# Optimization experiments

Hardware: AMD Instinct MI355X
Metric: run time of the kernel (lower is better)

Reference implementation:

```python
import jax, jax.numpy as jnp
import numpy as np

B, S, D, H = 2, 2048, 1024, 16
HD = D // H  # 64
MASK_VAL = -10000.0


def setup_inputs() -> dict:
    key = jax.random.key(0)
    ks = jax.random.split(key, 8)
    sc = 0.02
    q_features = jax.random.normal(ks[0], (B, S, D), jnp.float32)
    kv_features = jax.random.normal(ks[1], (B, S, D), jnp.float32)
    # causal mask, broadcastable (1,1,S,S)
    mask = jnp.tril(jnp.ones((S, S), jnp.bool_))[None, None]
    Wq = jax.random.normal(ks[2], (D, D), jnp.float32) * sc
    bq = jnp.zeros((D,), jnp.float32)
    Wkv = jax.random.normal(ks[3], (D, 2 * D), jnp.float32) * sc
    bkv = jnp.zeros((2 * D,), jnp.float32)
    Wp = jax.random.normal(ks[4], (D, D), jnp.float32) * sc
    bp = jnp.zeros((D,), jnp.float32)
    return {"q_features": q_features, "kv_features": kv_features, "mask": mask,
            "Wq": Wq, "bq": bq, "Wkv": Wkv, "bkv": bkv, "Wp": Wp, "bp": bp}


def _split_heads(t):
    # (B,S,D) -> (B,H,S,HD)
    return t.reshape(B, S, H, HD).transpose(0, 2, 1, 3)


def reference(q_features, kv_features, mask, Wq, bq, Wkv, bkv, Wp, bp):
    query = q_features @ Wq + bq            # (B,S,D)
    kv = kv_features @ Wkv + bkv            # (B,S,2D)
    key, value = jnp.split(kv, 2, axis=-1)
    q = _split_heads(query)                 # (B,H,S,HD)
    k = _split_heads(key)
    v = _split_heads(value)
    scores = jnp.einsum('bhqd,bhkd->bhqk', q, k) / jnp.sqrt(jnp.float32(HD))
    scores = jnp.where(mask, scores, jnp.asarray(MASK_VAL, scores.dtype))
    attn = jax.nn.softmax(scores, axis=-1)  # (B,H,S,S)
    out = jnp.einsum('bhqk,bhkd->bhqd', attn, v)
    out = out.transpose(0, 2, 1, 3).reshape(B, S, D)  # merge heads
    return out @ Wp + bp
```

## Files before the change

kernel.cpp:

```cpp
#include <hip/hip_runtime.h>

typedef unsigned short u16;
typedef unsigned int u32;
typedef __attribute__((ext_vector_type(4))) unsigned short us4;
typedef __attribute__((ext_vector_type(8))) unsigned short us8;
typedef __attribute__((ext_vector_type(4))) short s16x4;
typedef __attribute__((ext_vector_type(8))) __bf16 bf16x8;
typedef __attribute__((ext_vector_type(4))) float floatx4;

#define S_ 2048
#define D_ 1024
#define QSC 0.18033688f

__device__ __forceinline__ float b2f(u16 u) {
  unsigned v = ((unsigned)u) << 16;
  return __builtin_bit_cast(float, v);
}
__device__ __forceinline__ u16 f2bf(float f) {
  unsigned u = __builtin_bit_cast(unsigned, f);
  unsigned r = (u + 0x7fffu + ((u >> 16) & 1u)) >> 16;
  return (u16)r;
}
__device__ __forceinline__ u16 f2bf_rhu(float f) {
  return (u16)((__builtin_bit_cast(unsigned, f) + 0x8000u) >> 16);
}

typedef const __attribute__((address_space(1))) u32* gas_t;
typedef __attribute__((address_space(3))) u32* las_t;
__device__ __forceinline__ void gload16(const u16* g, u16* l) {
  __builtin_amdgcn_global_load_lds((gas_t)g, (las_t)l, 16, 0, 0);
}

#define PBAR()                                   \
  {                                              \
    __builtin_amdgcn_sched_barrier(0);           \
    asm volatile("" ::: "memory");               \
    __builtin_amdgcn_s_barrier();                \
    asm volatile("" ::: "memory");               \
    __builtin_amdgcn_sched_barrier(0);           \
  }
#define WAITVM(N) asm volatile("s_waitcnt vmcnt(" #N ")" ::: "memory")

__global__ __launch_bounds__(256) void prep(
    const float* __restrict__ qf, const float* __restrict__ kvf,
    const float* __restrict__ Wq, const float* __restrict__ Wkv,
    const float* __restrict__ Wp, u16* __restrict__ qa, u16* __restrict__ kva,
    u16* __restrict__ Wqt, u16* __restrict__ Wkvt, u16* __restrict__ Wpt) {
  int bid = blockIdx.x, tid = threadIdx.x;
  if (bid < 4096) {
    const float* src = (bid < 2048) ? qf : kvf;
    u16* dst = (bid < 2048) ? qa : kva;
    size_t i = ((size_t)(bid & 2047) * 256 + tid) * 8;
    floatx4 a = *(const floatx4*)(src + i);
    floatx4 b = *(const floatx4*)(src + i + 4);
    us8 r;
#pragma unroll
    for (int j = 0; j < 4; j++) { r[j] = f2bf(a[j]); r[4 + j] = f2bf(b[j]); }
    *(us8*)(dst + i) = r;
  } else {
    int t = bid - 4096;
    const float* src; u16* dst; int R, C;
    if (t < 1024)      { src = Wq;  dst = Wqt;  R = 1024; C = 1024; }
    else if (t < 3072) { t -= 1024; src = Wkv; dst = Wkvt; R = 1024; C = 2048; }
    else               { t -= 3072; src = Wp;  dst = Wpt;  R = 1024; C = 1024; }
    int bx = t % (C >> 5), by = t / (C >> 5);
    __shared__ u16 tile[32][33];
    int tx = tid & 31, ty = tid >> 5;
    int x = bx * 32 + tx;
    for (int i = ty; i < 32; i += 8)
      tile[i][tx] = f2bf(src[(size_t)(by * 32 + i) * C + x]);
    __syncthreads();
    int r = tid >> 3, c4 = tid & 7;
    us4 v;
#pragma unroll
    for (int j = 0; j < 4; j++) v[j] = tile[c4 * 4 + j][r];
    *(us4*)&dst[(size_t)(bx * 32 + r) * R + by * 32 + c4 * 4] = v;
  }
}

template <int MODE>
__device__ __forceinline__ void gemm256(
    const u16* __restrict__ A, const u16* __restrict__ Bt,
    const float* __restrict__ bias, void* __restrict__ C0,
    u16* __restrict__ C1, int N, int m0, int n0, u16* smem, float cscale) {
  int tid = threadIdx.x;
  int w = tid >> 6, lane = tid & 63;
  int quad = lane >> 4, l16 = lane & 15;
  int wr = w >> 2, wc = w & 3;

  int srow = w * 32 + (lane >> 2);
  int gchunk = ((lane & 3) ^ ((lane >> 3) & 3)) << 3;
  const u16* Asrc = A + (size_t)(m0 + srow) * 1024 + gchunk;
  const u16* Bsrc = Bt + (size_t)(n0 + srow) * 1024 + gchunk;
  u16* Adst = smem + w * 1024;
  u16* Bdst = smem + 32768 + w * 1024;

  int swz = (quad ^ ((l16 >> 1) & 3)) << 3;
  int aoff = (wr * 128 + l16) * 32 + swz;
  int boff = 32768 + (wc * 64 + l16) * 32 + swz;

  floatx4 acc[8][4] = {};

#define STG(t)                                                 \
  {                                                            \
    int s_ = (t) & 3;                                          \
    gload16(Asrc + (t) * 32, Adst + s_ * 8192);                \
    gload16(Asrc + (t) * 32 + 16384, Adst + s_ * 8192 + 512);  \
    gload16(Bsrc + (t) * 32, Bdst + s_ * 8192);                \
    gload16(Bsrc + (t) * 32 + 16384, Bdst + s_ * 8192 + 512);  \
  }

  STG(0); STG(1); STG(2);
  WAITVM(8);
  PBAR();

#pragma unroll 1
  for (int t = 0; t < 32; t++) {
    int so = (t & 3) * 8192;
    bf16x8 af[8], bf[4];
#pragma unroll
    for (int mf = 0; mf < 8; mf++)
      af[mf] = __builtin_bit_cast(bf16x8,
          *(const us8*)&smem[so + aoff + mf * 512]);
#pragma unroll
    for (int nf = 0; nf < 4; nf++)
      bf[nf] = __builtin_bit_cast(bf16x8,
          *(const us8*)&smem[so + boff + nf * 512]);
    if (t < 29) STG(t + 3);
    __builtin_amdgcn_s_setprio(1);
#pragma unroll
    for (int mf = 0; mf < 8; mf++)
#pragma unroll
      for (int nf = 0; nf < 4; nf++)
        acc[mf][nf] = __builtin_amdgcn_mfma_f32_16x16x32_bf16(
            af[mf], bf[nf], acc[mf][nf], 0, 0, 0);
    __builtin_amdgcn_s_setprio(0);
    if (t < 29)      { WAITVM(8); }
    else if (t == 29){ WAITVM(4); }
    else if (t == 30){ WAITVM(0); }
    if (t < 31) PBAR();
  }
#undef STG

#pragma unroll
  for (int mf = 0; mf < 8; mf++) {
#pragma unroll
    for (int nf = 0; nf < 4; nf++) {
      int col = n0 + wc * 64 + nf * 16 + l16;
      int rowq = m0 + wr * 128 + mf * 16 + quad * 4;
      float bv = bias[col];
      if (MODE == 0) {
        u16* o = (u16*)C0;
#pragma unroll
        for (int r = 0; r < 4; r++)
          o[(size_t)(rowq + r) * N + col] = f2bf((acc[mf][nf][r] + bv) * cscale);
      } else {
        if (col < 1024) {
          u16* o = (u16*)C0;
#pragma unroll
          for (int r = 0; r < 4; r++)
            o[(size_t)(rowq + r) * 1024 + col] = f2bf(acc[mf][nf][r] + bv);
        } else {
          int vcol = col - 1024;
          int b = rowq >> 11, s0 = rowq & 2047;
          us4 pv;
#pragma unroll
          for (int r = 0; r < 4; r++) pv[r] = f2bf(acc[mf][nf][r] + bv);
          *(us4*)&C1[((size_t)(b * 1024 + vcol)) * (size_t)S_ + s0] = pv;
        }
      }
    }
  }
}

__global__ __launch_bounds__(512, 2) void gemm_qkv(
    const u16* __restrict__ qa, const u16* __restrict__ kva,
    const u16* __restrict__ Wqt, const u16* __restrict__ Wkvt,
    const float* __restrict__ bq, const float* __restrict__ bkv,
    u16* __restrict__ Qb, u16* __restrict__ Kb, u16* __restrict__ Vt) {
  __shared__ __align__(16) u16 smem[65536];
  int bid = blockIdx.x;
  int work = (bid & 7) * 24 + (bid >> 3);
  if (work < 64) {
    gemm256<0>(qa, Wqt, bq, Qb, nullptr, 1024,
               (work >> 2) * 256, (work & 3) * 256, smem, QSC);
  } else {
    int lb = work - 64;
    gemm256<2>(kva, Wkvt, bkv, Kb, Vt, 2048,
               (lb >> 3) * 256, (lb & 7) * 256, smem, 1.0f);
  }
}

template <int TM, int TN, int MODE>
__device__ __forceinline__ void gemm4w(
    const u16* __restrict__ A, const u16* __restrict__ Bt,
    const float* __restrict__ bias, void* __restrict__ C0,
    u16* __restrict__ C1, int N, int m0, int n0, u16* smem, float cscale) {
  constexpr int MF = TM / 32, NF = TN / 32;
  constexpr int ASZ = TM * 64;
  constexpr int SLOT = (TM + TN) * 64;
  int tid = threadIdx.x;
  int w = tid >> 6, lane = tid & 63;
  int quad = lane >> 4, l16 = lane & 15;
  int wr = w >> 1, wc = w & 1;

  int gch = ((lane & 7) ^ ((lane >> 3) & 7)) << 3;
  const u16* Ag = A + (size_t)(m0 + w * (TM / 4) + (lane >> 3)) * 1024 + gch;
  const u16* Bg = Bt + (size_t)(n0 + w * (TN / 4) + (lane >> 3)) * 1024 + gch;
  u16* Adst = smem + w * (TM / 4) * 64;
  u16* Bdst = smem + ASZ + w * (TN / 4) * 64;

  int ab = (wr * (TM / 2) + l16) * 64;
  int bb = ASZ + (wc * (TN / 2) + l16) * 64;
  int xk0 = (quad ^ (l16 & 7)) << 3;
  int xk1 = ((4 + quad) ^ (l16 & 7)) << 3;

  floatx4 acc[MF][NF] = {};

#define STAGE4(tn, s_)                                                  \
  {                                                                     \
    _Pragma("unroll") for (int i = 0; i < MF; i++)                      \
      gload16(Ag + (size_t)(tn) * 64 + (size_t)i * 8192,                \
              Adst + (s_) * SLOT + i * 512);                            \
    _Pragma("unroll") for (int i = 0; i < NF; i++)                      \
      gload16(Bg + (size_t)(tn) * 64 + (size_t)i * 8192,                \
              Bdst + (s_) * SLOT + i * 512);                            \
  }

#define COMPUTE4(SOFF)                                                  \
  {                                                                     \
    _Pragma("unroll") for (int kk = 0; kk < 2; kk++) {                  \
      int xk = kk ? xk1 : xk0;                                          \
      bf16x8 bfr[NF];                                                   \
      _Pragma("unroll") for (int nf = 0; nf < NF; nf++)                 \
        bfr[nf] = __builtin_bit_cast(bf16x8,                            \
            *(const us8*)&smem[(SOFF) + bb + nf * 1024 + xk]);          \
      _Pragma("unroll") for (int mf = 0; mf < MF; mf++) {               \
        bf16x8 afr = __builtin_bit_cast(bf16x8,                         \
            *(const us8*)&smem[(SOFF) + ab + mf * 1024 + xk]);          \
        _Pragma("unroll") for (int nf = 0; nf < NF; nf++)               \
          acc[mf][nf] = __builtin_amdgcn_mfma_f32_16x16x32_bf16(        \
              afr, bfr[nf], acc[mf][nf], 0, 0, 0);                      \
      }                                                                 \
    }                                                                   \
  }

  STAGE4(0, 0);
  WAITVM(0);
  PBAR();
#pragma unroll 1
  for (int t = 0; t < 16; t += 2) {
    STAGE4(t + 1, 1);
    COMPUTE4(0);
    WAITVM(0);
    PBAR();
    if (t + 2 < 16) STAGE4(t + 2, 0);
    COMPUTE4(SLOT);
    WAITVM(0);
    PBAR();
  }

#undef STAGE4
#undef COMPUTE4

#pragma unroll
  for (int mf = 0; mf < MF; mf++) {
#pragma unroll
    for (int nf = 0; nf < NF; nf++) {
      int col = n0 + wc * (TN / 2) + nf * 16 + l16;
      int rowq = m0 + wr * (TM / 2) + mf * 16 + quad * 4;
      float bv = bias[col];
      if (MODE == 0) {
        u16* o = (u16*)C0;
#pragma unroll
        for (int r = 0; r < 4; r++)
          o[(size_t)(rowq + r) * N + col] = f2bf((acc[mf][nf][r] + bv) * cscale);
      } else if (MODE == 1) {
        float* o = (float*)C0;
#pragma unroll
        for (int r = 0; r < 4; r++)
          o[(size_t)(rowq + r) * N + col] = acc[mf][nf][r] + bv;
      } else {
        if (col < 1024) {
          u16* o = (u16*)C0;
#pragma unroll
          for (int r = 0; r < 4; r++)
            o[(size_t)(rowq + r) * 1024 + col] = f2bf(acc[mf][nf][r] + bv);
        } else {
          int vcol = col - 1024;
          int b = rowq >> 11, s0 = rowq & 2047;
          us4 pv;
#pragma unroll
          for (int r = 0; r < 4; r++) pv[r] = f2bf(acc[mf][nf][r] + bv);
          *(us4*)&C1[((size_t)(b * 1024 + vcol)) * (size_t)S_ + s0] = pv;
        }
      }
    }
  }
}

__global__ __launch_bounds__(256, 3) void gemm_out(
    const u16* __restrict__ AO, const u16* __restrict__ Wpt,
    const float* __restrict__ bp, float* __restrict__ out) {
  __shared__ __align__(16) u16 smem[24576];
  int work = (blockIdx.x & 7) * 64 + (blockIdx.x >> 3);
  gemm4w<128, 64, 1>(AO, Wpt, bp, out, nullptr, 1024,
                     (work >> 4) * 128, (work & 15) * 64, smem, 1.0f);
}

__global__ __launch_bounds__(512, 4) void attn_fwd(
    const u16* __restrict__ Q, const u16* __restrict__ Kb,
    const u16* __restrict__ Vt, u16* __restrict__ O,
    u16* __restrict__ Opart, float* __restrict__ ml) {
  __shared__ __align__(16) u16 sm[16384];
  int tid  = threadIdx.x;
  int w    = tid >> 6, lane = tid & 63;
  int quad = lane >> 4, l16 = lane & 15;
  int bh = blockIdx.x, b = bh >> 4, h = bh & 15;
  int y = blockIdx.y;

  static const signed char yt_[12] = {7,7,3,6,6,5,5,2,4,4,1,0};
  static const signed char yh_[12] = {0,1,-1,0,1,0,1,-1,0,1,-1,-1};
  int t = yt_[y], hh = yh_[y];
  bool split = hh >= 0;
  int kb0, kb1;
  if (split) { kb0 = hh ? (2 * t + 2) : 0; kb1 = hh ? (4 * t + 4) : (2 * t + 2); }
  else       { kb0 = 0; kb1 = 4 * t + 4; }
  int n = kb1 - kb0;

  const size_t row0 = (size_t)b * S_;
  const u16* Kg = Kb + row0 * D_ + h * 64;
  const u16* Vg = Vt + ((size_t)b * 1024 + h * 64) * S_;

  int qlo = t * 256 + w * 32;
  int dkb = qlo >> 6;
  int qgb = (w & 1) * 32;

  const u16* qp = Q + (row0 + qlo + l16) * D_ + h * 64 + quad * 8;
  bf16x8 aq[2][2];
  aq[0][0] = __builtin_bit_cast(bf16x8, *(const us8*)(qp));
  aq[0][1] = __builtin_bit_cast(bf16x8, *(const us8*)(qp + 32));
  aq[1][0] = __builtin_bit_cast(bf16x8, *(const us8*)(qp + (size_t)16 * D_));
  aq[1][1] = __builtin_bit_cast(bf16x8, *(const us8*)(qp + (size_t)16 * D_ + 32));

  floatx4 o_[2][4] = {};
  floatx4 l_acc[2] = {};
  const s16x4 ones4 = {0x3F80, 0x3F80, 0x3F80, 0x3F80};

  int srow = tid >> 3, c8 = tid & 7;
  int woff = srow * 64 + ((c8 ^ (srow & 7)) << 3);
  u16* smK = sm;
  u16* smV = sm + 8192;

  const u16* Kp = Kg + (size_t)(kb0 * 64 + srow) * D_ + c8 * 8;
  const u16* Vp = Vg + (size_t)srow * S_ + kb0 * 64 + c8 * 8;
  us8 pk = *(const us8*)Kp, pv = *(const us8*)Vp;
  *(us8*)&smK[woff] = pk;
  *(us8*)&smV[woff] = pv;
  if (n > 1) {
    Kp += (size_t)64 * D_; Vp += 64;
    pk = *(const us8*)Kp; pv = *(const us8*)Vp;
  }
  __syncthreads();

  for (int i = 0; i < n; i++) {
    int cur = i & 1;
    int kb = kb0 + i;
    if (i + 1 < n) {
      int nxt = (cur ^ 1) * 4096;
      *(us8*)&smK[nxt + woff] = pk;
      *(us8*)&smV[nxt + woff] = pv;
      if (i + 2 < n) {
        Kp += (size_t)64 * D_; Vp += 64;
        pk = *(const us8*)Kp; pv = *(const us8*)Vp;
      }
    }
    if (kb <= dkb) {
      const u16* Ksb = smK + cur * 4096;
      const u16* Vsb = smV + cur * 4096;

      floatx4 s[2][4] = {};
      __builtin_amdgcn_s_setprio(1);
#pragma unroll
      for (int kk = 0; kk < 2; kk++)
#pragma unroll
        for (int nt = 0; nt < 4; nt++) {
          us8 kf = *(const us8*)&Ksb[(nt * 16 + l16) * 64 +
                                     (((kk * 4 + quad) ^ (l16 & 7)) << 3)];
          bf16x8 kfb = __builtin_bit_cast(bf16x8, kf);
          s[0][nt] = __builtin_amdgcn_mfma_f32_16x16x32_bf16(
              kfb, aq[0][kk], s[0][nt], 0, 0, 0);
          s[1][nt] = __builtin_amdgcn_mfma_f32_16x16x32_bf16(
              kfb, aq[1][kk], s[1][nt], 0, 0, 0);
        }
      __builtin_amdgcn_s_setprio(0);

      if (kb == dkb) {
#pragma unroll
        for (int hf = 0; hf < 2; hf++) {
          int qg = qgb + hf * 16 + l16;
#pragma unroll
          for (int nt = 0; nt < 4; nt++)
#pragma unroll
            for (int r = 0; r < 4; r++)
              if (nt * 16 + quad * 4 + r > qg) s[hf][nt][r] = -1e5f;
        }
      }

      s16x4 pb[2][4];
#pragma unroll
      for (int hf = 0; hf < 2; hf++)
#pragma unroll
        for (int nt = 0; nt < 4; nt++)
#pragma unroll
          for (int r = 0; r < 4; r++)
            pb[hf][nt][r] = (short)f2bf_rhu(__builtin_amdgcn_exp2f(s[hf][nt][r]));

      __builtin_amdgcn_s_setprio(1);
#pragma unroll
      for (int nt = 0; nt < 4; nt++) {
        l_acc[0] = __builtin_amdgcn_mfma_f32_16x16x16bf16_1k(ones4, pb[0][nt], l_acc[0], 0, 0, 0);
        l_acc[1] = __builtin_amdgcn_mfma_f32_16x16x16bf16_1k(ones4, pb[1][nt], l_acc[1], 0, 0, 0);
#pragma unroll
        for (int mt = 0; mt < 4; mt++) {
          int hd = mt * 16 + l16;
          int chunk = nt * 2 + (quad >> 1);
          us4 vf = *(const us4*)&Vsb[hd * 64 + ((chunk ^ (l16 & 7)) << 3) + (quad & 1) * 4];
          s16x4 vb = __builtin_bit_cast(s16x4, vf);
          o_[0][mt] = __builtin_amdgcn_mfma_f32_16x16x16bf16_1k(
              vb, pb[0][nt], o_[0][mt], 0, 0, 0);
          o_[1][mt] = __builtin_amdgcn_mfma_f32_16x16x16bf16_1k(
              vb, pb[1][nt], o_[1][mt], 0, 0, 0);
        }
      }
      __builtin_amdgcn_s_setprio(0);
    }
    __syncthreads();
  }

  if (!split) {
#pragma unroll
    for (int hf = 0; hf < 2; hf++) {
      float rl = __builtin_amdgcn_rcpf(l_acc[hf][0]);
      size_t orow = (row0 + qlo + hf * 16 + l16) * D_ + h * 64;
#pragma unroll
      for (int mt = 0; mt < 4; mt++) {
        us4 ov;
#pragma unroll
        for (int r = 0; r < 4; r++) ov[r] = f2bf(o_[hf][mt][r] * rl);
        *(us4*)&O[orow + mt * 16 + quad * 4] = ov;
      }
    }
  } else {
    int part = (t - 4) * 2 + hh;
    u16* op = Opart + ((size_t)(bh * 8 + part)) * 16384;
#pragma unroll
    for (int hf = 0; hf < 2; hf++) {
      int rloc = w * 32 + hf * 16 + l16;
#pragma unroll
      for (int mt = 0; mt < 4; mt++) {
        us4 ov;
#pragma unroll
        for (int r = 0; r < 4; r++) ov[r] = f2bf(o_[hf][mt][r]);
        *(us4*)&op[rloc * 64 + mt * 16 + quad * 4] = ov;
      }
      if (quad == 0)
        ml[(size_t)(bh * 8 + part) * 256 + rloc] = l_acc[hf][0];
    }
  }
}

__global__ __launch_bounds__(256) void combine(
    const u16* __restrict__ Opart, const float* __restrict__ ml,
    u16* __restrict__ O) {
  int bh = blockIdx.x, b = bh >> 4, h = bh & 15;
  int t = 4 + blockIdx.y;
  int p0 = bh * 8 + (t - 4) * 2;
  const u16* o1 = Opart + (size_t)p0 * 16384;
  const u16* o2 = o1 + 16384;
  int row = threadIdx.x;
  float l1 = ml[(size_t)p0 * 256 + row];
  float l2 = ml[(size_t)(p0 + 1) * 256 + row];
  float inv = __builtin_amdgcn_rcpf(l1 + l2);
  size_t orow = ((size_t)b * S_ + t * 256 + row) * D_ + h * 64;
#pragma unroll
  for (int v = 0; v < 8; v++) {
    us8 x1 = *(const us8*)&o1[row * 64 + v * 8];
    us8 x2 = *(const us8*)&o2[row * 64 + v * 8];
    us8 out;
#pragma unroll
    for (int j = 0; j < 8; j++)
      out[j] = f2bf((b2f(x1[j]) + b2f(x2[j])) * inv);
    *(us8*)&O[orow + v * 8] = out;
  }
}

extern "C" void kernel_launch(void* const* d_in, const int* in_sizes, int n_in,
                              void* d_out, int out_size, void* d_ws, size_t ws_size,
                              hipStream_t stream) {
  const float* qf  = (const float*)d_in[0];
  const float* kvf = (const float*)d_in[1];
  const float* Wq  = (const float*)d_in[3];
  const float* bq  = (const float*)d_in[4];
  const float* Wkv = (const float*)d_in[5];
  const float* bkv = (const float*)d_in[6];
  const float* Wp  = (const float*)d_in[7];
  const float* bp  = (const float*)d_in[8];

  char* ws = (char*)d_ws;
  const size_t MB = 1048576;
  u16*   kva  = (u16*)(ws);
  u16*   AO   = (u16*)(ws);
  u16*   Kbp  = (u16*)(ws + 8 * MB);
  u16*   Vtp  = (u16*)(ws + 16 * MB);
  u16*   Wqt  = (u16*)(ws + 24 * MB);
  float* mlp  = (float*)(ws + 24 * MB);
  u16*   Wkvt = (u16*)(ws + 26 * MB);
  u16*   Wpt  = (u16*)(ws + 30 * MB);
  u16*   qa    = (u16*)d_out;
  u16*   Opart = (u16*)d_out;
  u16*   Qb    = (u16*)d_out + (size_t)4 * 1048576;

  prep<<<8192, 256, 0, stream>>>(qf, kvf, Wq, Wkv, Wp, qa, kva, Wqt, Wkvt, Wpt);
  gemm_qkv<<<192, 512, 0, stream>>>(qa, kva, Wqt, Wkvt, bq, bkv, Qb, Kbp, Vtp);
  attn_fwd<<<dim3(32, 12), 512, 0, stream>>>(Qb, Kbp, Vtp, AO, Opart, mlp);
  combine<<<dim3(32, 4), 256, 0, stream>>>(Opart, mlp, AO);
  gemm_out<<<512, 256, 0, stream>>>(AO, Wpt, bp, (float*)d_out);
}
```

Baseline: 205.4 us.

## Rewrite output projection GEMM with 4-stage K=32 pipeline and single barrier

Replaces the templated double-buffered 64-wide-K GEMM used for the output projection with a dedicated kernel core. It uses 32-wide K tiles in a 4-slot LDS ring with three loads in flight, and waits on the vector-memory counter with a nonzero count so only one barrier is needed per step. MFMA issue is wrapped in raised wave priority, and launch bounds drop to 2 blocks per CU. The aim is to hide global-load latency better in the small output GEMM, at the cost of more, smaller K steps with fewer MFMAs per barrier.

```diff
diff --git a/kernel.cpp b/kernel.cpp
--- a/kernel.cpp
+++ b/kernel.cpp
@@ -191,121 +191,87 @@
   }
 }
 
-template <int TM, int TN, int MODE>
-__device__ __forceinline__ void gemm4w(
+__device__ __forceinline__ void gemm_out_core(
     const u16* __restrict__ A, const u16* __restrict__ Bt,
-    const float* __restrict__ bias, void* __restrict__ C0,
-    u16* __restrict__ C1, int N, int m0, int n0, u16* smem, float cscale) {
-  constexpr int MF = TM / 32, NF = TN / 32;
-  constexpr int ASZ = TM * 64;
-  constexpr int SLOT = (TM + TN) * 64;
+    const float* __restrict__ bias, float* __restrict__ C,
+    int m0, int n0, u16* smem) {
   int tid = threadIdx.x;
   int w = tid >> 6, lane = tid & 63;
   int quad = lane >> 4, l16 = lane & 15;
   int wr = w >> 1, wc = w & 1;
 
-  int gch = ((lane & 7) ^ ((lane >> 3) & 7)) << 3;
-  const u16* Ag = A + (size_t)(m0 + w * (TM / 4) + (lane >> 3)) * 1024 + gch;
-  const u16* Bg = Bt + (size_t)(n0 + w * (TN / 4) + (lane >> 3)) * 1024 + gch;
-  u16* Adst = smem + w * (TM / 4) * 64;
-  u16* Bdst = smem + ASZ + w * (TN / 4) * 64;
-
-  int ab = (wr * (TM / 2) + l16) * 64;
-  int bb = ASZ + (wc * (TN / 2) + l16) * 64;
-  int xk0 = (quad ^ (l16 & 7)) << 3;
-  int xk1 = ((4 + quad) ^ (l16 & 7)) << 3;
-
-  floatx4 acc[MF][NF] = {};
-
-#define STAGE4(tn, s_)                                                  \
-  {                                                                     \
-    _Pragma("unroll") for (int i = 0; i < MF; i++)                      \
-      gload16(Ag + (size_t)(tn) * 64 + (size_t)i * 8192,                \
-              Adst + (s_) * SLOT + i * 512);                            \
-    _Pragma("unroll") for (int i = 0; i < NF; i++)                      \
-      gload16(Bg + (size_t)(tn) * 64 + (size_t)i * 8192,                \
-              Bdst + (s_) * SLOT + i * 512);                            \
-  }
-
-#define COMPUTE4(SOFF)                                                  \
-  {                                                                     \
-    _Pragma("unroll") for (int kk = 0; kk < 2; kk++) {                  \
-      int xk = kk ? xk1 : xk0;                                          \
-      bf16x8 bfr[NF];                                                   \
-      _Pragma("unroll") for (int nf = 0; nf < NF; nf++)                 \
-        bfr[nf] = __builtin_bit_cast(bf16x8,                            \
-            *(const us8*)&smem[(SOFF) + bb + nf * 1024 + xk]);          \
-      _Pragma("unroll") for (int mf = 0; mf < MF; mf++) {               \
-        bf16x8 afr = __builtin_bit_cast(bf16x8,                         \
-            *(const us8*)&smem[(SOFF) + ab + mf * 1024 + xk]);          \
-        _Pragma("unroll") for (int nf = 0; nf < NF; nf++)               \
-          acc[mf][nf] = __builtin_amdgcn_mfma_f32_16x16x32_bf16(        \
-              afr, bfr[nf], acc[mf][nf], 0, 0, 0);                      \
-      }                                                                 \
-    }                                                                   \
-  }
-
-  STAGE4(0, 0);
-  WAITVM(0);
+  int gchunk = ((lane & 3) ^ ((lane >> 3) & 3)) << 3;
+  const u16* Ag = A + (size_t)(m0 + w * 32 + (lane >> 2)) * 1024 + gchunk;
+  const u16* Bg = Bt + (size_t)(n0 + w * 16 + (lane >> 2)) * 1024 + gchunk;
+  u16* Adst = smem + w * 1024;
+  u16* Bdst = smem + 4096 + w * 512;
+
+  int swz = (quad ^ ((l16 >> 1) & 3)) << 3;
+  int aoff = (wr * 64 + l16) * 32 + swz;
+  int boff = 4096 + (wc * 32 + l16) * 32 + swz;
+
+  floatx4 acc[4][2] = {};
+
+#define STGO(t)                                                \
+  {                                                            \
+    int s_ = (t) & 3;                                          \
+    gload16(Ag + (t) * 32, Adst + s_ * 6144);                  \
+    gload16(Ag + (t) * 32 + 16384, Adst + s_ * 6144 + 512);    \
+    gload16(Bg + (t) * 32, Bdst + s_ * 6144);                  \
+  }
+
+  STGO(0); STGO(1); STGO(2);
+  WAITVM(6);
   PBAR();
+
 #pragma unroll 1
-  for (int t = 0; t < 16; t += 2) {
-    STAGE4(t + 1, 1);
-    COMPUTE4(0);
-    WAITVM(0);
-    PBAR();
-    if (t + 2 < 16) STAGE4(t + 2, 0);
-    COMPUTE4(SLOT);
-    WAITVM(0);
-    PBAR();
-  }
-
-#undef STAGE4
-#undef COMPUTE4
-
-#pragma unroll
-  for (int mf = 0; mf < MF; mf++) {
-#pragma unroll
-    for (int nf = 0; nf < NF; nf++) {
-      int col = n0 + wc * (TN / 2) + nf * 16 + l16;
-      int rowq = m0 + wr * (TM / 2) + mf * 16 + quad * 4;
+  for (int t = 0; t < 32; t++) {
+    int so = (t & 3) * 6144;
+    bf16x8 af[4], bf[2];
+#pragma unroll
+    for (int mf = 0; mf < 4; mf++)
+      af[mf] = __builtin_bit_cast(bf16x8,
+          *(const us8*)&smem[so + aoff + mf * 512]);
+#pragma unroll
+    for (int nf = 0; nf < 2; nf++)
+      bf[nf] = __builtin_bit_cast(bf16x8,
+          *(const us8*)&smem[so + boff + nf * 512]);
+    if (t < 29) STGO(t + 3);
+    __builtin_amdgcn_s_setprio(1);
+#pragma unroll
+    for (int mf = 0; mf < 4; mf++)
+#pragma unroll
+      for (int nf = 0; nf < 2; nf++)
+        acc[mf][nf] = __builtin_amdgcn_mfma_f32_16x16x32_bf16(
+            af[mf], bf[nf], acc[mf][nf], 0, 0, 0);
+    __builtin_amdgcn_s_setprio(0);
+    if (t < 29)      { WAITVM(6); }
+    else if (t == 29){ WAITVM(3); }
+    else if (t == 30){ WAITVM(0); }
+    if (t < 31) PBAR();
+  }
+#undef STGO
+
+#pragma unroll
+  for (int mf = 0; mf < 4; mf++) {
+#pragma unroll
+    for (int nf = 0; nf < 2; nf++) {
+      int col = n0 + wc * 32 + nf * 16 + l16;
+      int rowq = m0 + wr * 64 + mf * 16 + quad * 4;
       float bv = bias[col];
-      if (MODE == 0) {
-        u16* o = (u16*)C0;
-#pragma unroll
-        for (int r = 0; r < 4; r++)
-          o[(size_t)(rowq + r) * N + col] = f2bf((acc[mf][nf][r] + bv) * cscale);
-      } else if (MODE == 1) {
-        float* o = (float*)C0;
-#pragma unroll
-        for (int r = 0; r < 4; r++)
-          o[(size_t)(rowq + r) * N + col] = acc[mf][nf][r] + bv;
-      } else {
-        if (col < 1024) {
-          u16* o = (u16*)C0;
-#pragma unroll
-          for (int r = 0; r < 4; r++)
-            o[(size_t)(rowq + r) * 1024 + col] = f2bf(acc[mf][nf][r] + bv);
-        } else {
-          int vcol = col - 1024;
-          int b = rowq >> 11, s0 = rowq & 2047;
-          us4 pv;
-#pragma unroll
-          for (int r = 0; r < 4; r++) pv[r] = f2bf(acc[mf][nf][r] + bv);
-          *(us4*)&C1[((size_t)(b * 1024 + vcol)) * (size_t)S_ + s0] = pv;
-        }
-      }
-    }
-  }
-}
-
-__global__ __launch_bounds__(256, 3) void gemm_out(
+#pragma unroll
+      for (int r = 0; r < 4; r++)
+        C[(size_t)(rowq + r) * 1024 + col] = acc[mf][nf][r] + bv;
+    }
+  }
+}
+
+__global__ __launch_bounds__(256, 2) void gemm_out(
     const u16* __restrict__ AO, const u16* __restrict__ Wpt,
     const float* __restrict__ bp, float* __restrict__ out) {
   __shared__ __align__(16) u16 smem[24576];
   int work = (blockIdx.x & 7) * 64 + (blockIdx.x >> 3);
-  gemm4w<128, 64, 1>(AO, Wpt, bp, out, nullptr, 1024,
-                     (work >> 4) * 128, (work & 15) * 64, smem, 1.0f);
+  gemm_out_core(AO, Wpt, bp, out, (work >> 4) * 128, (work & 15) * 64, smem);
 }
 
 __global__ __launch_bounds__(512, 4) void attn_fwd(
```

Result: no change. 208.4 us, median of 2 (+1.5%).
